# Performance work log

Hardware: AMD Instinct MI355X
Metric: run time of the kernel (lower is better)

The kernel has to match this reference:

```python
import jax, jax.numpy as jnp
import numpy as np

N_NODES = 50000
N_EDGES = 200000
D_FEAT = 512
D_HID = 1024


def setup_inputs() -> dict:
    key = jax.random.key(0)
    k_x, k_s, k_d, k_w1, k_w2 = jax.random.split(key, 5)
    x = jax.random.normal(k_x, (N_NODES, D_FEAT), dtype=jnp.float32)
    src = jax.random.randint(k_s, (N_EDGES,), 0, N_NODES, dtype=jnp.int64)
    dst = jax.random.randint(k_d, (N_EDGES,), 0, N_NODES, dtype=jnp.int64)
    # MLP params: Linear(2d -> hidden), ReLU, Linear(hidden -> 1)
    W1 = jax.random.normal(k_w1, (2 * D_FEAT, D_HID), dtype=jnp.float32) * (1.0 / np.sqrt(2 * D_FEAT))
    b1 = jnp.zeros((D_HID,), dtype=jnp.float32)
    W2 = jax.random.normal(k_w2, (D_HID, 1), dtype=jnp.float32) * (1.0 / np.sqrt(D_HID))
    b2 = jnp.zeros((1,), dtype=jnp.float32)
    return {"x": x, "src": src, "dst": dst, "W1": W1, "b1": b1, "W2": W2, "b2": b2}


def reference(x, src, dst, W1, b1, W2, b2):
    # Per-edge gather of src/dst node embeddings, concat along feature dim
    h = jnp.concatenate([x[src], x[dst]], axis=1)          # [E, 2d]
    h = jax.nn.relu(h @ W1 + b1)                            # [E, hidden]
    score = h @ W2 + b2                                     # [E, 1]
    return score
```

## Files before the change

kernel.cpp:

```cpp
#include <hip/hip_runtime.h>
#include <cstdint>
#include <cstddef>

typedef __attribute__((ext_vector_type(8))) short short8;
typedef __attribute__((ext_vector_type(4))) float f32x4;

#define D_FEAT 512
#define D_HID  1024
#define NCOL   2048
#define NCHUNK 32

__device__ __forceinline__ unsigned short f2bf(float f) {
    unsigned u = __builtin_bit_cast(unsigned, f);
    u += 0x7FFFu + ((u >> 16) & 1u);
    return (unsigned short)(u >> 16);
}

#define NCAST 12500

__global__ __launch_bounds__(256) void prep_kernel(const float* __restrict__ x,
                                                   unsigned short* __restrict__ xb,
                                                   const float* __restrict__ W1,
                                                   unsigned short* __restrict__ w1t,
                                                   int n) {
    if ((int)blockIdx.x < NCAST) {
        int i = (blockIdx.x * 256 + threadIdx.x) * 8;
        if (i >= n) return;
        const float4* xp = (const float4*)(x + i);
        float4 a = xp[0], b = xp[1];
        short8 o;
        o[0] = (short)f2bf(a.x); o[1] = (short)f2bf(a.y);
        o[2] = (short)f2bf(a.z); o[3] = (short)f2bf(a.w);
        o[4] = (short)f2bf(b.x); o[5] = (short)f2bf(b.y);
        o[6] = (short)f2bf(b.z); o[7] = (short)f2bf(b.w);
        *(short8*)(xb + i) = o;
    } else {
        __shared__ float tile[32][33];
        const int bid2 = blockIdx.x - NCAST;
        const int half = bid2 >> 9;
        const int kb   = ((bid2 >> 5) & 15) * 32;
        const int nb   = (bid2 & 31) * 32;
        const int tx = threadIdx.x & 31, ty = threadIdx.x >> 5;
        #pragma unroll
        for (int i = 0; i < 32; i += 8)
            tile[ty + i][tx] = W1[(size_t)(half * 512 + kb + ty + i) * 1024 + nb + tx];
        __syncthreads();
        #pragma unroll
        for (int i = 0; i < 32; i += 8)
            w1t[(size_t)(half * 1024 + nb + ty + i) * 512 + kb + tx] = f2bf(tile[tx][ty + i]);
    }
}

#define BM 128
#define BN 128
#define BK 64
#define GM 32

__global__ __launch_bounds__(256, 2) void gemm_uv_kernel(
    const unsigned short* __restrict__ xb,
    const unsigned short* __restrict__ w1t,
    const float* __restrict__ b1,
    unsigned char* __restrict__ qUV,
    float* __restrict__ scales,
    int M, int MB)
{
    __shared__ __align__(16) unsigned short smem[16384];
    unsigned short* sA = smem;
    unsigned short* sB = smem + 8192;

    const int NB = NCOL / BN;
    int bid = blockIdx.x;
    int g    = bid / (GM * NB);
    int rem  = bid - g * (GM * NB);
    int base = g * GM;
    int gm   = MB - base; if (gm > GM) gm = GM;
    int mb   = base + rem % gm;
    int nb   = rem / gm;
    const int m0 = mb * BM;
    const int n0 = nb * BN;

    const int tid  = threadIdx.x;
    const int wave = tid >> 6;
    const int lane = tid & 63;
    const int q    = lane >> 4;
    const int l15  = lane & 15;
    const int wm   = (wave >> 1) * 64;
    const int wn   = (wave & 1) * 64;

    const int ar = lane >> 3;
    const int ac = ((lane & 7) ^ ar) * 8;

    const int swz = l15 & 7;
    const int c0 = (q ^ swz) * 8;
    const int c1 = ((q ^ swz) ^ 4) * 8;

    float b1v[4];
    #pragma unroll
    for (int nt = 0; nt < 4; ++nt) {
        int n = n0 + wn + nt * 16 + l15;
        b1v[nt] = (n < D_HID) ? b1[n] : 0.f;
    }

    f32x4 acc[4][4];
    #pragma unroll
    for (int i = 0; i < 4; ++i)
        #pragma unroll
        for (int j = 0; j < 4; ++j)
            acc[i][j] = (f32x4){b1v[j], b1v[j], b1v[j], b1v[j]};

    #pragma unroll 1
    for (int kt = 0; kt < 8; ++kt) {
        const int k0 = kt * BK;
        __syncthreads();
        #pragma unroll
        for (int i = 0; i < 4; ++i) {
            int slot = wave * 4 + i;
            int row  = slot * 8 + ar;
            int m    = m0 + row; if (m >= M) m = M - 1;
            __builtin_amdgcn_global_load_lds(
                (const __attribute__((address_space(1))) void*)(xb + (size_t)m * D_FEAT + k0 + ac),
                (__attribute__((address_space(3))) void*)(sA + slot * 512),
                16, 0, 0);
        }
        #pragma unroll
        for (int i = 0; i < 4; ++i) {
            int slot = wave * 4 + i;
            int row  = slot * 8 + ar;
            __builtin_amdgcn_global_load_lds(
                (const __attribute__((address_space(1))) void*)(w1t + (size_t)(n0 + row) * D_FEAT + k0 + ac),
                (__attribute__((address_space(3))) void*)(sB + slot * 512),
                16, 0, 0);
        }
        __syncthreads();
        {
            short8 a[4], b[4];
            #pragma unroll
            for (int mt = 0; mt < 4; ++mt)
                a[mt] = *(const short8*)(sA + (wm + mt * 16 + l15) * 64 + c0);
            #pragma unroll
            for (int nt = 0; nt < 4; ++nt)
                b[nt] = *(const short8*)(sB + (wn + nt * 16 + l15) * 64 + c0);
            #pragma unroll
            for (int mt = 0; mt < 4; ++mt)
                #pragma unroll
                for (int nt = 0; nt < 4; ++nt)
                    acc[mt][nt] = __builtin_amdgcn_mfma_f32_16x16x32_bf16(a[mt], b[nt], acc[mt][nt], 0, 0, 0);
            #pragma unroll
            for (int mt = 0; mt < 4; ++mt)
                a[mt] = *(const short8*)(sA + (wm + mt * 16 + l15) * 64 + c1);
            #pragma unroll
            for (int nt = 0; nt < 4; ++nt)
                b[nt] = *(const short8*)(sB + (wn + nt * 16 + l15) * 64 + c1);
            #pragma unroll
            for (int mt = 0; mt < 4; ++mt)
                #pragma unroll
                for (int nt = 0; nt < 4; ++nt)
                    acc[mt][nt] = __builtin_amdgcn_mfma_f32_16x16x32_bf16(a[mt], b[nt], acc[mt][nt], 0, 0, 0);
        }
    }

    float msc[4], minv[4];
    #pragma unroll
    for (int mt = 0; mt < 4; ++mt) {
        float m_ = 1e-30f;
        #pragma unroll
        for (int nt = 0; nt < 4; ++nt)
            #pragma unroll
            for (int r = 0; r < 4; ++r)
                m_ = fmaxf(m_, fabsf(acc[mt][nt][r]));
        #pragma unroll
        for (int off = 1; off < 64; off <<= 1)
            m_ = fmaxf(m_, __shfl_xor(m_, off));
        msc[mt]  = m_ * (1.0f / 127.0f);
        minv[mt] = 127.0f * __builtin_amdgcn_rcpf(m_);
    }

    __syncthreads();
    unsigned char* ep8 = (unsigned char*)smem + wave * 4096;
    const float MAGIC = 12583040.0f;
    #pragma unroll
    for (int mt = 0; mt < 4; ++mt)
        #pragma unroll
        for (int nt = 0; nt < 4; ++nt)
            #pragma unroll
            for (int r = 0; r < 4; ++r) {
                float f = fmaf(acc[mt][nt][r], minv[mt], MAGIC);
                ep8[(mt * 16 + q * 4 + r) * 64 + nt * 16 + l15] =
                    (unsigned char)__builtin_bit_cast(unsigned, f);
            }
    const int chunk = (n0 + wn) >> 6;
    {
        int srow = m0 + wm + q * 16 + l15;
        if (srow < M) scales[(size_t)srow * NCHUNK + chunk] = msc[q];
    }
    #pragma unroll
    for (int i = 0; i < 4; ++i) {
        int flat = i * 64 + lane;
        int r   = flat >> 2;
        int c16 = (flat & 3) * 16;
        int m   = m0 + wm + r;
        if (m < M) {
            int4 v = *(const int4*)(ep8 + r * 64 + c16);
            *(int4*)(qUV + (size_t)m * NCOL + n0 + wn + c16) = v;
        }
    }
}

__global__ __launch_bounds__(256) void edge_score_kernel(
    const unsigned char* __restrict__ qUV,
    const float* __restrict__ scales,
    const int* __restrict__ src, const int* __restrict__ dst,
    const float* __restrict__ W2, const float* __restrict__ b2,
    float* __restrict__ out, int E)
{
    const int wave = threadIdx.x >> 6;
    const int lane = threadIdx.x & 63;
    const int gw = blockIdx.x * 4 + wave;
    const int ebase = gw * 4;
    if (ebase >= E) return;

    const float4* wp = (const float4*)(W2 + lane * 16);
    float4 wa = wp[0], wb = wp[1], wcv = wp[2], wd = wp[3];
    float w[16] = {wa.x, wa.y, wa.z, wa.w, wb.x, wb.y, wb.z, wb.w,
                   wcv.x, wcv.y, wcv.z, wcv.w, wd.x, wd.y, wd.z, wd.w};
    const float bias = b2[0];
    const int ch = lane >> 2;

    #pragma unroll
    for (int p = 0; p < 2; ++p) {
        const int e0 = ebase + p * 2;
        if (e0 < E) {
            const int e1 = e0 + 1;
            const bool has1 = (e1 < E);

            const int s0 = src[e0];
            const int d0 = dst[e0];
            const int s1 = has1 ? src[e1] : s0;
            const int d1 = has1 ? dst[e1] : d0;

            uint4 qu0 = *(const uint4*)(qUV + (size_t)s0 * NCOL + lane * 16);
            uint4 qv0 = *(const uint4*)(qUV + (size_t)d0 * NCOL + D_HID + lane * 16);
            uint4 qu1 = *(const uint4*)(qUV + (size_t)s1 * NCOL + lane * 16);
            uint4 qv1 = *(const uint4*)(qUV + (size_t)d1 * NCOL + D_HID + lane * 16);
            float su0 = scales[(size_t)s0 * NCHUNK + ch];
            float sv0 = scales[(size_t)d0 * NCHUNK + 16 + ch];
            float su1 = scales[(size_t)s1 * NCHUNK + ch];
            float sv1 = scales[(size_t)d1 * NCHUNK + 16 + ch];
            float cc0 = -128.0f * (su0 + sv0);
            float cc1 = -128.0f * (su1 + sv1);

            const unsigned* u0w = (const unsigned*)&qu0; const unsigned* v0w = (const unsigned*)&qv0;
            const unsigned* u1w = (const unsigned*)&qu1; const unsigned* v1w = (const unsigned*)&qv1;

            float acc0 = 0.f, acc1 = 0.f;
            #pragma unroll
            for (int dw = 0; dw < 4; ++dw) {
                #pragma unroll
                for (int b = 0; b < 4; ++b) {
                    int k = dw * 4 + b;
                    float ub0 = (float)((u0w[dw] >> (8 * b)) & 0xFFu);
                    float vb0 = (float)((v0w[dw] >> (8 * b)) & 0xFFu);
                    float h0 = fmaf(ub0, su0, fmaf(vb0, sv0, cc0));
                    acc0 = fmaf(fmaxf(h0, 0.f), w[k], acc0);
                    float ub1 = (float)((u1w[dw] >> (8 * b)) & 0xFFu);
                    float vb1 = (float)((v1w[dw] >> (8 * b)) & 0xFFu);
                    float h1 = fmaf(ub1, su1, fmaf(vb1, sv1, cc1));
                    acc1 = fmaf(fmaxf(h1, 0.f), w[k], acc1);
                }
            }
            #pragma unroll
            for (int off = 1; off < 64; off <<= 1) {
                acc0 += __shfl_xor(acc0, off);
                acc1 += __shfl_xor(acc1, off);
            }
            if (lane == 0) out[e0] = acc0 + bias;
            if (lane == 1 && has1) out[e1] = acc1 + bias;
        }
    }
}

extern "C" void kernel_launch(void* const* d_in, const int* in_sizes, int n_in,
                              void* d_out, int out_size, void* d_ws, size_t ws_size,
                              hipStream_t stream) {
    const float* x   = (const float*)d_in[0];
    const int*   src = (const int*)d_in[1];
    const int*   dst = (const int*)d_in[2];
    const float* W1  = (const float*)d_in[3];
    const float* b1  = (const float*)d_in[4];
    const float* W2  = (const float*)d_in[5];
    const float* b2  = (const float*)d_in[6];
    float* out = (float*)d_out;

    const int M = in_sizes[0] / D_FEAT;
    const int E = in_sizes[1];

    char* ws = (char*)d_ws;
    unsigned char*  qUV    = (unsigned char*)ws;
    float*          scales = (float*)(ws + (size_t)M * NCOL);
    unsigned short* xb     = (unsigned short*)(ws + (size_t)M * NCOL + (size_t)M * NCHUNK * 4);
    unsigned short* w1t    = (unsigned short*)(ws + (size_t)M * NCOL + (size_t)M * NCHUNK * 4
                                                  + (size_t)M * D_FEAT * 2);

    const int nx = M * D_FEAT;
    prep_kernel<<<NCAST + 1024, 256, 0, stream>>>(x, xb, W1, w1t, nx);
    const int MB = (M + BM - 1) / BM;
    gemm_uv_kernel<<<MB * (NCOL / BN), 256, 0, stream>>>(xb, w1t, b1, qUV, scales, M, MB);
    edge_score_kernel<<<(E + 15) / 16, 256, 0, stream>>>(qUV, scales, src, dst, W2, b2, out, E);
}
```

Measured before the change: 332.4 us.

## Swizzle GEMM epilogue LDS staging and batch all four edge gathers per wave

The GEMM epilogue now XOR-swizzles the 16-byte column slot by row group when staging int8 results in shared memory, to cut bank conflicts on the byte writes and the vector reads. The edge-score kernel now loads the indices, quantized rows and scales for all four edges of a wave up front, then runs the compute and shuffle reductions for the four edges together. This gives more memory-level parallelism on the random gathers than the previous two-at-a-time loop, at the cost of higher register pressure.

```diff
diff --git a/kernel.cpp b/kernel.cpp
--- a/kernel.cpp
+++ b/kernel.cpp
@@ -185,7 +185,7 @@
             #pragma unroll
             for (int r = 0; r < 4; ++r) {
                 float f = fmaf(acc[mt][nt][r], minv[mt], MAGIC);
-                ep8[(mt * 16 + q * 4 + r) * 64 + nt * 16 + l15] =
+                ep8[(mt * 16 + q * 4 + r) * 64 + ((nt ^ q) * 16) + l15] =
                     (unsigned char)__builtin_bit_cast(unsigned, f);
             }
     const int chunk = (n0 + wn) >> 6;
@@ -197,11 +197,11 @@
     for (int i = 0; i < 4; ++i) {
         int flat = i * 64 + lane;
         int r   = flat >> 2;
-        int c16 = (flat & 3) * 16;
+        int cI  = flat & 3;
         int m   = m0 + wm + r;
         if (m < M) {
-            int4 v = *(const int4*)(ep8 + r * 64 + c16);
-            *(int4*)(qUV + (size_t)m * NCOL + n0 + wn + c16) = v;
+            int4 v = *(const int4*)(ep8 + r * 64 + ((cI ^ ((r >> 2) & 3)) * 16));
+            *(int4*)(qUV + (size_t)m * NCOL + n0 + wn + cI * 16) = v;
         }
     }
 }
@@ -219,64 +219,68 @@
     const int ebase = gw * 4;
     if (ebase >= E) return;
 
+    const int ch = lane >> 2;
+
+    int sidx[4], didx[4];
+    #pragma unroll
+    for (int p = 0; p < 4; ++p) {
+        int e  = ebase + p;
+        int ec = (e < E) ? e : (E - 1);
+        sidx[p] = src[ec];
+        didx[p] = dst[ec];
+    }
+
+    uint4 qu[4], qv[4];
+    #pragma unroll
+    for (int p = 0; p < 4; ++p) {
+        qu[p] = *(const uint4*)(qUV + (size_t)sidx[p] * NCOL + lane * 16);
+        qv[p] = *(const uint4*)(qUV + (size_t)didx[p] * NCOL + D_HID + lane * 16);
+    }
+    float su[4], sv[4];
+    #pragma unroll
+    for (int p = 0; p < 4; ++p) {
+        su[p] = scales[(size_t)sidx[p] * NCHUNK + ch];
+        sv[p] = scales[(size_t)didx[p] * NCHUNK + 16 + ch];
+    }
+
     const float4* wp = (const float4*)(W2 + lane * 16);
     float4 wa = wp[0], wb = wp[1], wcv = wp[2], wd = wp[3];
     float w[16] = {wa.x, wa.y, wa.z, wa.w, wb.x, wb.y, wb.z, wb.w,
                    wcv.x, wcv.y, wcv.z, wcv.w, wd.x, wd.y, wd.z, wd.w};
     const float bias = b2[0];
-    const int ch = lane >> 2;
-
-    #pragma unroll
-    for (int p = 0; p < 2; ++p) {
-        const int e0 = ebase + p * 2;
-        if (e0 < E) {
-            const int e1 = e0 + 1;
-            const bool has1 = (e1 < E);
-
-            const int s0 = src[e0];
-            const int d0 = dst[e0];
-            const int s1 = has1 ? src[e1] : s0;
-            const int d1 = has1 ? dst[e1] : d0;
-
-            uint4 qu0 = *(const uint4*)(qUV + (size_t)s0 * NCOL + lane * 16);
-            uint4 qv0 = *(const uint4*)(qUV + (size_t)d0 * NCOL + D_HID + lane * 16);
-            uint4 qu1 = *(const uint4*)(qUV + (size_t)s1 * NCOL + lane * 16);
-            uint4 qv1 = *(const uint4*)(qUV + (size_t)d1 * NCOL + D_HID + lane * 16);
-            float su0 = scales[(size_t)s0 * NCHUNK + ch];
-            float sv0 = scales[(size_t)d0 * NCHUNK + 16 + ch];
-            float su1 = scales[(size_t)s1 * NCHUNK + ch];
-            float sv1 = scales[(size_t)d1 * NCHUNK + 16 + ch];
-            float cc0 = -128.0f * (su0 + sv0);
-            float cc1 = -128.0f * (su1 + sv1);
-
-            const unsigned* u0w = (const unsigned*)&qu0; const unsigned* v0w = (const unsigned*)&qv0;
-            const unsigned* u1w = (const unsigned*)&qu1; const unsigned* v1w = (const unsigned*)&qv1;
-
-            float acc0 = 0.f, acc1 = 0.f;
-            #pragma unroll
-            for (int dw = 0; dw < 4; ++dw) {
-                #pragma unroll
-                for (int b = 0; b < 4; ++b) {
-                    int k = dw * 4 + b;
-                    float ub0 = (float)((u0w[dw] >> (8 * b)) & 0xFFu);
-                    float vb0 = (float)((v0w[dw] >> (8 * b)) & 0xFFu);
-                    float h0 = fmaf(ub0, su0, fmaf(vb0, sv0, cc0));
-                    acc0 = fmaf(fmaxf(h0, 0.f), w[k], acc0);
-                    float ub1 = (float)((u1w[dw] >> (8 * b)) & 0xFFu);
-                    float vb1 = (float)((v1w[dw] >> (8 * b)) & 0xFFu);
-                    float h1 = fmaf(ub1, su1, fmaf(vb1, sv1, cc1));
-                    acc1 = fmaf(fmaxf(h1, 0.f), w[k], acc1);
-                }
+
+    float cc[4], acc[4];
+    #pragma unroll
+    for (int p = 0; p < 4; ++p) {
+        cc[p]  = -128.0f * (su[p] + sv[p]);
+        acc[p] = 0.f;
+    }
+
+    #pragma unroll
+    for (int dw = 0; dw < 4; ++dw) {
+        #pragma unroll
+        for (int b = 0; b < 4; ++b) {
+            const int k = dw * 4 + b;
+            #pragma unroll
+            for (int p = 0; p < 4; ++p) {
+                const unsigned* uw = (const unsigned*)&qu[p];
+                const unsigned* vw = (const unsigned*)&qv[p];
+                float ub = (float)((uw[dw] >> (8 * b)) & 0xFFu);
+                float vb = (float)((vw[dw] >> (8 * b)) & 0xFFu);
+                float h  = fmaf(ub, su[p], fmaf(vb, sv[p], cc[p]));
+                acc[p] = fmaf(fmaxf(h, 0.f), w[k], acc[p]);
             }
-            #pragma unroll
-            for (int off = 1; off < 64; off <<= 1) {
-                acc0 += __shfl_xor(acc0, off);
-                acc1 += __shfl_xor(acc1, off);
-            }
-            if (lane == 0) out[e0] = acc0 + bias;
-            if (lane == 1 && has1) out[e1] = acc1 + bias;
-        }
-    }
+        }
+    }
+    #pragma unroll
+    for (int off = 1; off < 64; off <<= 1) {
+        #pragma unroll
+        for (int p = 0; p < 4; ++p)
+            acc[p] += __shfl_xor(acc[p], off);
+    }
+    #pragma unroll
+    for (int p = 0; p < 4; ++p)
+        if (lane == p && ebase + p < E) out[ebase + p] = acc[p] + bias;
 }
 
 extern "C" void kernel_launch(void* const* d_in, const int* in_sizes, int n_in,
```

Result: slower. 344.4 us (+3.6%).

## Fuse fp32-to-bf16 cast of x into GEMM A-tile load, swizzle epilogue LDS

Applied to the files above, without the earlier changes.

Drops the separate pass that turns x into bf16. The GEMM now loads fp32 rows of x into registers, converts them, and writes them into the swizzled LDS A tile, so the bf16 copy of x no longer makes a round trip through global memory. The epilogue's int8 staging buffer also gets an XOR swizzle to cut LDS bank conflicts. The trade-off is that x is read as fp32 once per N-block (16 times), doubling A-side traffic, and the async global_load_lds path for A becomes register loads followed by a barrier, which may hurt latency hiding.

```diff
diff --git a/kernel.cpp b/kernel.cpp
--- a/kernel.cpp
+++ b/kernel.cpp
@@ -16,39 +16,21 @@
     return (unsigned short)(u >> 16);
 }
 
-#define NCAST 12500
-
-__global__ __launch_bounds__(256) void prep_kernel(const float* __restrict__ x,
-                                                   unsigned short* __restrict__ xb,
-                                                   const float* __restrict__ W1,
-                                                   unsigned short* __restrict__ w1t,
-                                                   int n) {
-    if ((int)blockIdx.x < NCAST) {
-        int i = (blockIdx.x * 256 + threadIdx.x) * 8;
-        if (i >= n) return;
-        const float4* xp = (const float4*)(x + i);
-        float4 a = xp[0], b = xp[1];
-        short8 o;
-        o[0] = (short)f2bf(a.x); o[1] = (short)f2bf(a.y);
-        o[2] = (short)f2bf(a.z); o[3] = (short)f2bf(a.w);
-        o[4] = (short)f2bf(b.x); o[5] = (short)f2bf(b.y);
-        o[6] = (short)f2bf(b.z); o[7] = (short)f2bf(b.w);
-        *(short8*)(xb + i) = o;
-    } else {
-        __shared__ float tile[32][33];
-        const int bid2 = blockIdx.x - NCAST;
-        const int half = bid2 >> 9;
-        const int kb   = ((bid2 >> 5) & 15) * 32;
-        const int nb   = (bid2 & 31) * 32;
-        const int tx = threadIdx.x & 31, ty = threadIdx.x >> 5;
-        #pragma unroll
-        for (int i = 0; i < 32; i += 8)
-            tile[ty + i][tx] = W1[(size_t)(half * 512 + kb + ty + i) * 1024 + nb + tx];
-        __syncthreads();
-        #pragma unroll
-        for (int i = 0; i < 32; i += 8)
-            w1t[(size_t)(half * 1024 + nb + ty + i) * 512 + kb + tx] = f2bf(tile[tx][ty + i]);
-    }
+__global__ __launch_bounds__(256) void prep_kernel(const float* __restrict__ W1,
+                                                   unsigned short* __restrict__ w1t) {
+    __shared__ float tile[32][33];
+    const int bid2 = blockIdx.x;
+    const int half = bid2 >> 9;
+    const int kb   = ((bid2 >> 5) & 15) * 32;
+    const int nb   = (bid2 & 31) * 32;
+    const int tx = threadIdx.x & 31, ty = threadIdx.x >> 5;
+    #pragma unroll
+    for (int i = 0; i < 32; i += 8)
+        tile[ty + i][tx] = W1[(size_t)(half * 512 + kb + ty + i) * 1024 + nb + tx];
+    __syncthreads();
+    #pragma unroll
+    for (int i = 0; i < 32; i += 8)
+        w1t[(size_t)(half * 1024 + nb + ty + i) * 512 + kb + tx] = f2bf(tile[tx][ty + i]);
 }
 
 #define BM 128
@@ -57,7 +39,7 @@
 #define GM 32
 
 __global__ __launch_bounds__(256, 2) void gemm_uv_kernel(
-    const unsigned short* __restrict__ xb,
+    const float* __restrict__ x,
     const unsigned short* __restrict__ w1t,
     const float* __restrict__ b1,
     unsigned char* __restrict__ qUV,
@@ -94,6 +76,13 @@
     const int c0 = (q ^ swz) * 8;
     const int c1 = ((q ^ swz) ^ 4) * 8;
 
+    int rowAm[4];
+    #pragma unroll
+    for (int i = 0; i < 4; ++i) {
+        int m = m0 + (wave * 4 + i) * 8 + ar;
+        rowAm[i] = (m < M) ? m : (M - 1);
+    }
+
     float b1v[4];
     #pragma unroll
     for (int nt = 0; nt < 4; ++nt) {
@@ -111,16 +100,26 @@
     #pragma unroll 1
     for (int kt = 0; kt < 8; ++kt) {
         const int k0 = kt * BK;
+
+        float4 fa[4][2];
+        #pragma unroll
+        for (int i = 0; i < 4; ++i) {
+            const float4* xp = (const float4*)(x + (size_t)rowAm[i] * D_FEAT + k0 + ac);
+            fa[i][0] = xp[0];
+            fa[i][1] = xp[1];
+        }
+
         __syncthreads();
+
         #pragma unroll
         for (int i = 0; i < 4; ++i) {
             int slot = wave * 4 + i;
-            int row  = slot * 8 + ar;
-            int m    = m0 + row; if (m >= M) m = M - 1;
-            __builtin_amdgcn_global_load_lds(
-                (const __attribute__((address_space(1))) void*)(xb + (size_t)m * D_FEAT + k0 + ac),
-                (__attribute__((address_space(3))) void*)(sA + slot * 512),
-                16, 0, 0);
+            short8 o;
+            o[0] = (short)f2bf(fa[i][0].x); o[1] = (short)f2bf(fa[i][0].y);
+            o[2] = (short)f2bf(fa[i][0].z); o[3] = (short)f2bf(fa[i][0].w);
+            o[4] = (short)f2bf(fa[i][1].x); o[5] = (short)f2bf(fa[i][1].y);
+            o[6] = (short)f2bf(fa[i][1].z); o[7] = (short)f2bf(fa[i][1].w);
+            *(short8*)(sA + slot * 512 + lane * 8) = o;
         }
         #pragma unroll
         for (int i = 0; i < 4; ++i) {
@@ -185,7 +184,7 @@
             #pragma unroll
             for (int r = 0; r < 4; ++r) {
                 float f = fmaf(acc[mt][nt][r], minv[mt], MAGIC);
-                ep8[(mt * 16 + q * 4 + r) * 64 + nt * 16 + l15] =
+                ep8[(mt * 16 + q * 4 + r) * 64 + ((nt ^ q) * 16) + l15] =
                     (unsigned char)__builtin_bit_cast(unsigned, f);
             }
     const int chunk = (n0 + wn) >> 6;
@@ -197,11 +196,11 @@
     for (int i = 0; i < 4; ++i) {
         int flat = i * 64 + lane;
         int r   = flat >> 2;
-        int c16 = (flat & 3) * 16;
+        int cI  = flat & 3;
         int m   = m0 + wm + r;
         if (m < M) {
-            int4 v = *(const int4*)(ep8 + r * 64 + c16);
-            *(int4*)(qUV + (size_t)m * NCOL + n0 + wn + c16) = v;
+            int4 v = *(const int4*)(ep8 + r * 64 + ((cI ^ ((r >> 2) & 3)) * 16));
+            *(int4*)(qUV + (size_t)m * NCOL + n0 + wn + cI * 16) = v;
         }
     }
 }
@@ -297,13 +296,10 @@
     char* ws = (char*)d_ws;
     unsigned char*  qUV    = (unsigned char*)ws;
     float*          scales = (float*)(ws + (size_t)M * NCOL);
-    unsigned short* xb     = (unsigned short*)(ws + (size_t)M * NCOL + (size_t)M * NCHUNK * 4);
-    unsigned short* w1t    = (unsigned short*)(ws + (size_t)M * NCOL + (size_t)M * NCHUNK * 4
-                                                  + (size_t)M * D_FEAT * 2);
-
-    const int nx = M * D_FEAT;
-    prep_kernel<<<NCAST + 1024, 256, 0, stream>>>(x, xb, W1, w1t, nx);
+    unsigned short* w1t    = (unsigned short*)(ws + (size_t)M * NCOL + (size_t)M * NCHUNK * 4);
+
+    prep_kernel<<<1024, 256, 0, stream>>>(W1, w1t);
     const int MB = (M + BM - 1) / BM;
-    gemm_uv_kernel<<<MB * (NCOL / BN), 256, 0, stream>>>(xb, w1t, b1, qUV, scales, M, MB);
+    gemm_uv_kernel<<<MB * (NCOL / BN), 256, 0, stream>>>(x, w1t, b1, qUV, scales, M, MB);
     edge_score_kernel<<<(E + 15) / 16, 256, 0, stream>>>(qUV, scales, src, dst, W2, b2, out, E);
 }
```

New measurement: 357.3 us. +7.5%, slower.
